# Optimization experiments

Hardware: AMD Instinct MI355X
Metric: run time of the kernel (lower is better)

The kernel has to match this reference:

```python
import jax, jax.numpy as jnp
import numpy as np

IMG = 640
C = 80
K = 10
LB, LC = 7.5, 0.5
ALPHA_COST, BETA_COST = 0.5, 6.0
GAMMA, ALPHA = 2.0, 0.25
EPS = 1e-7
PI = 3.141592653589793


def xywh_to_xyxy(b):
    cx, cy, w, h = b[..., 0], b[..., 1], b[..., 2], b[..., 3]
    return jnp.stack([cx - w * 0.5, cy - h * 0.5, cx + w * 0.5, cy + h * 0.5], axis=-1)


def bbox_iou(box1, box2):
    # box1 [M,4], box2 [N,4] xyxy -> [M,N]
    area1 = jnp.clip(box1[:, 2] - box1[:, 0], 0) * jnp.clip(box1[:, 3] - box1[:, 1], 0)
    area2 = jnp.clip(box2[:, 2] - box2[:, 0], 0) * jnp.clip(box2[:, 3] - box2[:, 1], 0)
    ix1 = jnp.maximum(box1[:, None, 0], box2[None, :, 0])
    iy1 = jnp.maximum(box1[:, None, 1], box2[None, :, 1])
    ix2 = jnp.minimum(box1[:, None, 2], box2[None, :, 2])
    iy2 = jnp.minimum(box1[:, None, 3], box2[None, :, 3])
    inter = jnp.clip(ix2 - ix1, 0) * jnp.clip(iy2 - iy1, 0)
    union = area1[:, None] + area2[None, :] - inter + EPS
    return jnp.clip(inter / union, 0.0, 1.0)


def bbox_ciou(p, t):
    # elementwise [N,4] x [N,4] xyxy -> [N]
    px1, py1, px2, py2 = p[:, 0], p[:, 1], p[:, 2], p[:, 3]
    tx1, ty1, tx2, ty2 = t[:, 0], t[:, 1], t[:, 2], t[:, 3]
    pw = jnp.clip(px2 - px1, EPS)
    ph = jnp.clip(py2 - py1, EPS)
    tw = jnp.clip(tx2 - tx1, EPS)
    th = jnp.clip(ty2 - ty1, EPS)
    inter = jnp.clip(jnp.minimum(px2, tx2) - jnp.maximum(px1, tx1), 0) * \
            jnp.clip(jnp.minimum(py2, ty2) - jnp.maximum(py1, ty1), 0)
    union = pw * ph + tw * th - inter + EPS
    iou = inter / union
    cd = ((px1 + px2) * 0.5 - (tx1 + tx2) * 0.5) ** 2 + ((py1 + py2) * 0.5 - (ty1 + ty2) * 0.5) ** 2
    cw = jnp.maximum(px2, tx2) - jnp.minimum(px1, tx1)
    ch = jnp.maximum(py2, ty2) - jnp.minimum(py1, ty1)
    c2 = cw ** 2 + ch ** 2 + EPS
    v = (4.0 / PI ** 2) * (jnp.arctan(tw / th) - jnp.arctan(pw / ph)) ** 2
    alpha = jax.lax.stop_gradient(v / (v - iou + 1.0 + EPS))
    return iou - cd / c2 - alpha * v


def _decode(p, stride):
    # p: [B, A, S, S, E] -> box [B, A*S*S, 4] (xywh px), cls [B, A*S*S, C]
    B, A, S, _, E = p.shape
    tx, ty, tw, th = p[..., 0], p[..., 1], p[..., 2], p[..., 3]
    gy, gx = jnp.meshgrid(jnp.arange(S, dtype=p.dtype), jnp.arange(S, dtype=p.dtype), indexing='ij')
    gx = gx.reshape(1, 1, S, S)
    gy = gy.reshape(1, 1, S, S)
    px = (jax.nn.sigmoid(tx) * 2.0 - 0.5 + gx) * stride  # center_mode='v8'
    py = (jax.nn.sigmoid(ty) * 2.0 - 0.5 + gy) * stride
    pw = jax.nn.softplus(tw) * stride                      # wh_mode='softplus'
    ph = jax.nn.softplus(th) * stride
    box = jnp.stack([px, py, pw, ph], axis=-1).reshape(B, -1, 4)
    cls = p[..., 4:].reshape(B, -1, C)
    return box, cls


def _per_image(p_box, p_logits, gt, labels):
    # p_box [M,4] xywh, p_logits [M,C], gt [N,4] xyxy, labels [N]
    N = gt.shape[0]
    tcx = (gt[:, 0] + gt[:, 2]) * 0.5
    tcy = (gt[:, 1] + gt[:, 3]) * 0.5
    dist = (p_box[:, 0][:, None] - tcx[None, :]) ** 2 + (p_box[:, 1][:, None] - tcy[None, :]) ** 2  # [M,N]
    _, cand = jax.lax.top_k(-dist.T, K)       # [N,K] nearest anchors per target
    cand = cand.reshape(-1)                    # [N*K] (dups don't change the min)
    cand_box = p_box[cand]
    cand_logits = p_logits[cand]
    cls_score = jax.nn.sigmoid(cand_logits)[:, labels]          # [NK,N]
    iou = bbox_iou(xywh_to_xyxy(cand_box), gt)                  # [NK,N]
    cost = ALPHA_COST * (1.0 - cls_score) + BETA_COST * (1.0 - iou)
    matched = cand[jnp.argmin(cost, axis=0)]                    # [N]
    ciou = bbox_ciou(xywh_to_xyxy(p_box[matched]), gt)
    loss_box = LB * jnp.sum(1.0 - ciou) / N
    tgt = jnp.zeros_like(p_logits).at[matched, labels].set(1.0)  # [M,C]
    x = p_logits
    ce = jnp.maximum(x, 0) - x * tgt + jnp.log1p(jnp.exp(-jnp.abs(x)))
    pr = jax.nn.sigmoid(x)
    p_t = pr * tgt + (1 - pr) * (1 - tgt)
    fl = ce * (1 - p_t) ** GAMMA
    a_t = ALPHA * tgt + (1 - ALPHA) * (1 - tgt)
    loss_cls = LC * jnp.sum(a_t * fl) / N
    return loss_box + loss_cls


def _forward(p0, p1, p2, gt_boxes, labels):
    boxes, logits = [], []
    for p in (p0, p1, p2):
        S = p.shape[2]
        pb, pl = _decode(p, float(IMG) / S)
        boxes.append(pb)
        logits.append(pl)
    flat_boxes = jnp.concatenate(boxes, axis=1)    # [B, 8400, 4]
    flat_logits = jnp.concatenate(logits, axis=1)  # [B, 8400, C]
    per_img = jax.vmap(_per_image)(flat_boxes, flat_logits, gt_boxes, labels)  # [B]
    return jnp.mean(per_img)


def setup_inputs() -> dict:
    key = jax.random.key(0)
    k0, k1, k2, kc, kw, kl = jax.random.split(key, 6)
    B, N = 16, 60
    p0 = jax.random.normal(k0, (B, 1, 80, 80, 84), dtype=jnp.float32)
    p1 = jax.random.normal(k1, (B, 1, 40, 40, 84), dtype=jnp.float32)
    p2 = jax.random.normal(k2, (B, 1, 20, 20, 84), dtype=jnp.float32)
    c = jax.random.uniform(kc, (B, N, 2), minval=64.0, maxval=576.0)
    wh = jax.random.uniform(kw, (B, N, 2), minval=8.0, maxval=128.0)
    gt_boxes = jnp.concatenate([c - wh * 0.5, c + wh * 0.5], axis=-1).astype(jnp.float32)
    labels = jax.random.randint(kl, (B, N), 0, 80, dtype=jnp.int32)
    return {"p0": p0, "p1": p1, "p2": p2, "gt_boxes": gt_boxes, "labels": labels}


def reference(p0, p1, p2, gt_boxes, labels):
    return _forward(p0, p1, p2, gt_boxes, labels)
```

## Files before the change

### kernel.cpp

```cpp
#include <hip/hip_runtime.h>
#include <cfloat>
#include <math.h>

#define NB   16
#define NGT  60
#define NA   8400
#define KNN  10
#define NCAND (NGT*KNN)
#define EPSF 1e-7f
#define PIF  3.14159265358979f

#define FOCAL_BLOCKS  2100
#define SPARSE_BLOCKS 240
#define K1_BLOCKS (FOCAL_BLOCKS + SPARSE_BLOCKS)

#define NV0   2150400u
#define NV1    537600u
#define NV2    134400u
#define FOCAL_COUNT 2688000u

#define LOG2E 1.44269504088896341f
#define LN2   0.69314718055994531f

__device__ __forceinline__ float fexp2(float x){ return __builtin_amdgcn_exp2f(x); }
__device__ __forceinline__ float flog2(float x){ return __builtin_amdgcn_logf(x); }
__device__ __forceinline__ float frcp (float x){ return __builtin_amdgcn_rcpf(x); }

__device__ __forceinline__ float fsigm(float x){
  return frcp(1.0f + fexp2(-x*LOG2E));
}
__device__ __forceinline__ float fsoftplus(float x){
  float u = fexp2(-fabsf(x)*LOG2E);
  return fmaxf(x,0.f) + LN2*flog2(1.0f + u);
}
__device__ __forceinline__ float fbg(float x){
  float u = fexp2(fminf(-x*LOG2E, 126.0f));
  float t = frcp(1.0f + u);
  return (x + LN2*flog2(1.0f + u)) * t * t;
}

__device__ __forceinline__ float focal_fbg4(const float* __restrict__ p0,
                                            const float* __restrict__ p1,
                                            const float* __restrict__ p2, unsigned u){
  unsigned g = u / 20u;
  unsigned v = 21u*g + (u - 20u*g) + 1u;
  const float* p; unsigned vloc;
  if (v < NV0)          { p=p0; vloc = v; }
  else if (v < NV0+NV1) { p=p1; vloc = v - NV0; }
  else                  { p=p2; vloc = v - (NV0+NV1); }
  float4 x4 = *(const float4*)(p + (size_t)vloc*4u);
  return fbg(x4.x) + fbg(x4.y) + fbg(x4.z) + fbg(x4.w);
}

struct ARow { const float* q; float stf; int i, j; };
__device__ __forceinline__ ARow anchor_row(const float* p0,const float* p1,const float* p2,int img,int a){
  ARow r;
  if (a < 6400){ int l=a;      r.q = p0 + (size_t)(img*6400 + l)*84; r.stf= 8.f; r.i=l/80; r.j=l-80*r.i; }
  else if (a < 8000){ int l=a-6400; r.q = p1 + (size_t)(img*1600 + l)*84; r.stf=16.f; r.i=l/40; r.j=l-40*r.i; }
  else { int l=a-8000;         r.q = p2 + (size_t)(img*400  + l)*84; r.stf=32.f; r.i=l/20; r.j=l-20*r.i; }
  return r;
}
__device__ __forceinline__ float4 decode_box_xywh(const ARow& r){
  float4 x4 = *(const float4*)r.q;
  float px = (fsigm(x4.x)*2.f - 0.5f + (float)r.j)*r.stf;
  float py = (fsigm(x4.y)*2.f - 0.5f + (float)r.i)*r.stf;
  float pw = fsoftplus(x4.z)*r.stf;
  float ph = fsoftplus(x4.w)*r.stf;
  return make_float4(px,py,pw,ph);
}

__global__ __launch_bounds__(256) void k1_kernel(const float* __restrict__ p0,
                                                 const float* __restrict__ p1,
                                                 const float* __restrict__ p2,
                                                 const float* __restrict__ gt,
                                                 const int* __restrict__ labels,
                                                 int* __restrict__ cand,
                                                 unsigned long long* __restrict__ partials,
                                                 float* __restrict__ fsum){
  if (blockIdx.x < FOCAL_BLOCKS){
    __shared__ float sbuf[4];
    const unsigned S = FOCAL_BLOCKS*256u;
    unsigned u = blockIdx.x*256u + threadIdx.x;
    float s0 = focal_fbg4(p0,p1,p2, u);
    float s1 = focal_fbg4(p0,p1,p2, u +   S);
    float s2 = focal_fbg4(p0,p1,p2, u + 2*S);
    float s3 = focal_fbg4(p0,p1,p2, u + 3*S);
    float s4 = focal_fbg4(p0,p1,p2, u + 4*S);
    float sum = (((s0 + s1) + (s2 + s3)) + s4) * 0.75f;
    #pragma unroll
    for (int off=32; off>0; off>>=1) sum += __shfl_xor(sum, off);
    int wid = threadIdx.x >> 6;
    if ((threadIdx.x & 63) == 0) sbuf[wid] = sum;
    __syncthreads();
    if (threadIdx.x == 0) fsum[blockIdx.x] = sbuf[0]+sbuf[1]+sbuf[2]+sbuf[3];
    return;
  }

  int wid  = threadIdx.x >> 6;
  int lane = threadIdx.x & 63;
  int pair = (blockIdx.x - FOCAL_BLOCKS)*4 + wid;
  int img = pair / NGT, g = pair - img*NGT;
  const float* gb = gt + (size_t)(img*NGT + g)*4;
  float tcx = (gb[0]+gb[2])*0.5f, tcy = (gb[1]+gb[3])*0.5f;

  int jx0 = (int)(tcx * 0.125f),   iy0 = (int)(tcy * 0.125f);
  int jx1 = (int)(tcx * 0.0625f),  iy1 = (int)(tcy * 0.0625f);
  int jx2 = (int)(tcx * 0.03125f), iy2 = (int)(tcy * 0.03125f);

  float d0=FLT_MAX,d1=FLT_MAX,d2=FLT_MAX,d3=FLT_MAX;
  int   a0,a1,a2,a3;
  #pragma unroll
  for (int s=0; s<4; s++){
    int c = lane + 64*s;
    float dd = FLT_MAX; int aa = 9000000 + c;
    const float* p; int i, j, S, base, rowmul, valid = 1; float stf;
    if (c < 169)      { int r=c/13,  q=c-13*r;           i=iy0-6+r; j=jx0-6+q; S=80; base=0;    p=p0; rowmul=6400; stf= 8.f; }
    else if (c < 218) { int t=c-169; int r=t/7, q=t-7*r; i=iy1-3+r; j=jx1-3+q; S=40; base=6400; p=p1; rowmul=1600; stf=16.f; }
    else if (c < 243) { int t=c-218; int r=t/5, q=t-5*r; i=iy2-2+r; j=jx2-2+q; S=20; base=8000; p=p2; rowmul=400;  stf=32.f; }
    else { valid = 0; i=j=0; S=1; base=0; p=p0; rowmul=0; stf=0.f; }
    if (valid && i>=0 && i<S && j>=0 && j<S){
      int local = i*S + j;
      const float* q4 = p + (size_t)(img*rowmul + local)*84u;
      float2 xy = *(const float2*)q4;
      float px = (fsigm(xy.x)*2.f - 0.5f + (float)j)*stf;
      float py = (fsigm(xy.y)*2.f - 0.5f + (float)i)*stf;
      float dx=px-tcx, dy=py-tcy;
      dd = dx*dx + dy*dy;
      aa = base + local;
    }
    if (s==0){ d0=dd; a0=aa; } else if (s==1){ d1=dd; a1=aa; }
    else if (s==2){ d2=dd; a2=aa; } else { d3=dd; a3=aa; }
  }

  int anc_r[KNN];
  #pragma unroll
  for (int r=0; r<KNN; r++){
    float v = d0; int anc = a0;
    if (d1 < v || (d1==v && a1<anc)){ v=d1; anc=a1; }
    if (d2 < v || (d2==v && a2<anc)){ v=d2; anc=a2; }
    if (d3 < v || (d3==v && a3<anc)){ v=d3; anc=a3; }
    #pragma unroll
    for (int off=32; off>0; off>>=1){
      float v2 = __shfl_xor(v, off);
      int  A2 = __shfl_xor(anc, off);
      if (v2 < v || (v2==v && A2<anc)){ v=v2; anc=A2; }
    }
    if (a0==anc) d0=FLT_MAX;
    if (a1==anc) d1=FLT_MAX;
    if (a2==anc) d2=FLT_MAX;
    if (a3==anc) d3=FLT_MAX;
    anc_r[r] = anc;
    if (lane == 0) cand[(size_t)pair*KNN + r] = anc;
  }

  bool jv = (lane < NGT);
  float4 gbj = make_float4(0.f,0.f,0.f,0.f);
  int labj = 0;
  if (jv){
    gbj  = *(const float4*)(gt + (size_t)(img*NGT + lane)*4);
    labj = labels[img*NGT + lane];
  }
  float a2g = fmaxf(gbj.z-gbj.x,0.f)*fmaxf(gbj.w-gbj.y,0.f);
  unsigned long long best = ~0ull;
  #pragma unroll
  for (int r=0; r<KNN; r++){
    int a = anc_r[r];
    ARow ar = anchor_row(p0,p1,p2,img,a);
    float4 b = decode_box_xywh(ar);
    float bx1=b.x-b.z*0.5f, by1=b.y-b.w*0.5f, bx2=b.x+b.z*0.5f, by2=b.y+b.w*0.5f;
    float a1 = fmaxf(bx2-bx1,0.f)*fmaxf(by2-by1,0.f);
    float ix1=fmaxf(bx1,gbj.x), iy1=fmaxf(by1,gbj.y);
    float ix2=fminf(bx2,gbj.z), iy2=fminf(by2,gbj.w);
    float inter = fmaxf(ix2-ix1,0.f)*fmaxf(iy2-iy1,0.f);
    float uni = a1 + a2g - inter + EPSF;
    float iou = fminf(fmaxf(inter/uni,0.f),1.f);
    float lg = ar.q[4+labj];
    float cost = 0.5f*(1.f - fsigm(lg)) + 6.f*(1.f - iou);
    unsigned long long pk = ((unsigned long long)__float_as_uint(cost) << 32)
                          | (unsigned)(g*KNN + r);
    if (pk < best) best = pk;
  }
  if (jv) partials[((size_t)img*NGT + g)*NGT + lane] = best;
}

__global__ __launch_bounds__(1024) void k2_kernel(const unsigned long long* __restrict__ partials,
                                                  const int* __restrict__ cand,
                                                  const float* __restrict__ gt,
                                                  const int* __restrict__ labels,
                                                  const float* __restrict__ p0,
                                                  const float* __restrict__ p1,
                                                  const float* __restrict__ p2,
                                                  const float* __restrict__ fsum,
                                                  float* __restrict__ out){
  int tid = threadIdx.x;
  int wid = tid >> 6;
  int lane = tid & 63;
  __shared__ int sm[NB][NGT];
  __shared__ int sl[NB][NGT];
  __shared__ float wb[NB], wc[NB], wf[NB];
  int img = wid;
  if (lane < NGT){
    unsigned long long best = ~0ull;
    #pragma unroll 4
    for (int g2=0; g2<NGT; g2++){
      unsigned long long v = partials[((size_t)img*NGT + g2)*NGT + lane];
      if (v < best) best = v;
    }
    int slot = (int)(best & 0xffffffffull);
    sm[img][lane] = cand[img*NCAND + slot];
    sl[img][lane] = labels[img*NGT + lane];
  }
  __syncthreads();

  float local_box = 0.f, local_corr = 0.f;
  if (lane < NGT){
    int j = lane;
    int m = sm[img][j];
    ARow ar = anchor_row(p0,p1,p2,img,m);
    float4 pb = decode_box_xywh(ar);
    float px1=pb.x-pb.z*0.5f, py1=pb.y-pb.w*0.5f, px2=pb.x+pb.z*0.5f, py2=pb.y+pb.w*0.5f;
    const float* gb = gt + (size_t)(img*NGT + j)*4;
    float gx=gb[0], gy=gb[1], gz=gb[2], gw=gb[3];
    float pw=fmaxf(px2-px1,EPSF), ph=fmaxf(py2-py1,EPSF);
    float tw=fmaxf(gz-gx,EPSF),  th=fmaxf(gw-gy,EPSF);
    float inter = fmaxf(fminf(px2,gz)-fmaxf(px1,gx),0.f)*fmaxf(fminf(py2,gw)-fmaxf(py1,gy),0.f);
    float uni = pw*ph + tw*th - inter + EPSF;
    float iou = inter/uni;
    float dcx = (px1+px2)*0.5f - (gx+gz)*0.5f;
    float dcy = (py1+py2)*0.5f - (gy+gw)*0.5f;
    float cd = dcx*dcx + dcy*dcy;
    float cw = fmaxf(px2,gz) - fminf(px1,gx);
    float ch = fmaxf(py2,gw) - fminf(py1,gy);
    float c2 = cw*cw + ch*ch + EPSF;
    float dv = atanf(tw/th) - atanf(pw/ph);
    float v  = (4.f/(PIF*PIF))*dv*dv;
    float alpha = v/(v - iou + 1.f + EPSF);
    float ciou = iou - cd/c2 - alpha*v;
    local_box = 1.f - ciou;

    int lab = sl[img][j];
    bool dup = false;
    for (int j2=0; j2<j; j2++)
      if (sm[img][j2]==m && sl[img][j2]==lab){ dup=true; break; }
    if (!dup){
      float x = ar.q[4+lab];
      float s  = fsigm(x);
      float u  = fexp2(-fabsf(x)*LOG2E);
      float lt = LN2*flog2(1.0f + u);
      float sp_pos = fmaxf(-x,0.f) + lt;
      float sp_neg = fmaxf( x,0.f) + lt;
      local_corr = 0.25f*sp_pos*(1.f-s)*(1.f-s) - 0.75f*sp_neg*s*s;
    }
  }
  float local_f = fsum[tid] + fsum[tid + 1024];
  if (tid < FOCAL_BLOCKS - 2048) local_f += fsum[tid + 2048];
  #pragma unroll
  for (int off=32; off>0; off>>=1){
    local_box  += __shfl_xor(local_box,  off);
    local_corr += __shfl_xor(local_corr, off);
    local_f    += __shfl_xor(local_f,    off);
  }
  if (lane == 0){ wb[wid]=local_box; wc[wid]=local_corr; wf[wid]=local_f; }
  __syncthreads();
  if (tid == 0){
    float sb=0.f, sc=0.f, sf=0.f;
    #pragma unroll
    for (int k=0;k<NB;k++){ sb+=wb[k]; sc+=wc[k]; sf+=wf[k]; }
    out[0] = (7.5f*sb + 0.5f*(sf + sc)) / (60.f*16.f);
  }
}

extern "C" void kernel_launch(void* const* d_in, const int* in_sizes, int n_in,
                              void* d_out, int out_size, void* d_ws, size_t ws_size,
                              hipStream_t stream){
  const float* p0 = (const float*)d_in[0];
  const float* p1 = (const float*)d_in[1];
  const float* p2 = (const float*)d_in[2];
  const float* gt = (const float*)d_in[3];
  const int* labels = (const int*)d_in[4];
  float* out = (float*)d_out;

  unsigned long long* partials = (unsigned long long*)d_ws;
  float* fsum = (float*)((char*)d_ws + (size_t)NB*NGT*NGT*8);
  int*   cand = (int*)((char*)fsum + FOCAL_BLOCKS*sizeof(float));

  k1_kernel<<<K1_BLOCKS, 256, 0, stream>>>(p0, p1, p2, gt, labels, cand, partials, fsum);
  k2_kernel<<<1, 1024, 0, stream>>>(partials, cand, gt, labels, p0, p1, p2, fsum, out);
}
```

Measured before the change: 47.54 us.

## Pack anchor index into cost key, pre-reduce per block, schedule sparse blocks first

The anchor index is encoded into the low bits of the packed cost key, so the cand buffer and its indirect lookup go away. Each sparse block reduces its four GT rows in shared memory before writing, which cuts the partials that k2 scans per image from 60 to 15. Sparse blocks are moved to the start of the grid so they are dispatched before the focal blocks and the assignment tail overlaps the streaming work. The 14-bit anchor field holds indices up to 8400, and tie-breaking stays in the same order because the slot bits sit above the anchor bits.

```diff
diff --git a/kernel.cpp b/kernel.cpp
--- a/kernel.cpp
+++ b/kernel.cpp
@@ -10,9 +10,9 @@
 #define EPSF 1e-7f
 #define PIF  3.14159265358979f
 
+#define SPARSE_BLOCKS 240
 #define FOCAL_BLOCKS  2100
-#define SPARSE_BLOCKS 240
-#define K1_BLOCKS (FOCAL_BLOCKS + SPARSE_BLOCKS)
+#define K1_BLOCKS (SPARSE_BLOCKS + FOCAL_BLOCKS)
 
 #define NV0   2150400u
 #define NV1    537600u
@@ -74,13 +74,12 @@
                                                  const float* __restrict__ p2,
                                                  const float* __restrict__ gt,
                                                  const int* __restrict__ labels,
-                                                 int* __restrict__ cand,
                                                  unsigned long long* __restrict__ partials,
                                                  float* __restrict__ fsum){
-  if (blockIdx.x < FOCAL_BLOCKS){
+  if (blockIdx.x >= SPARSE_BLOCKS){
     __shared__ float sbuf[4];
     const unsigned S = FOCAL_BLOCKS*256u;
-    unsigned u = blockIdx.x*256u + threadIdx.x;
+    unsigned u = (blockIdx.x - SPARSE_BLOCKS)*256u + threadIdx.x;
     float s0 = focal_fbg4(p0,p1,p2, u);
     float s1 = focal_fbg4(p0,p1,p2, u +   S);
     float s2 = focal_fbg4(p0,p1,p2, u + 2*S);
@@ -92,13 +91,13 @@
     int wid = threadIdx.x >> 6;
     if ((threadIdx.x & 63) == 0) sbuf[wid] = sum;
     __syncthreads();
-    if (threadIdx.x == 0) fsum[blockIdx.x] = sbuf[0]+sbuf[1]+sbuf[2]+sbuf[3];
+    if (threadIdx.x == 0) fsum[blockIdx.x - SPARSE_BLOCKS] = sbuf[0]+sbuf[1]+sbuf[2]+sbuf[3];
     return;
   }
 
   int wid  = threadIdx.x >> 6;
   int lane = threadIdx.x & 63;
-  int pair = (blockIdx.x - FOCAL_BLOCKS)*4 + wid;
+  int pair = blockIdx.x*4 + wid;
   int img = pair / NGT, g = pair - img*NGT;
   const float* gb = gt + (size_t)(img*NGT + g)*4;
   float tcx = (gb[0]+gb[2])*0.5f, tcy = (gb[1]+gb[3])*0.5f;
@@ -150,7 +149,6 @@
     if (a2==anc) d2=FLT_MAX;
     if (a3==anc) d3=FLT_MAX;
     anc_r[r] = anc;
-    if (lane == 0) cand[(size_t)pair*KNN + r] = anc;
   }
 
   bool jv = (lane < NGT);
@@ -177,14 +175,24 @@
     float lg = ar.q[4+labj];
     float cost = 0.5f*(1.f - fsigm(lg)) + 6.f*(1.f - iou);
     unsigned long long pk = ((unsigned long long)__float_as_uint(cost) << 32)
-                          | (unsigned)(g*KNN + r);
+                          | ((unsigned long long)(unsigned)(g*KNN + r) << 14)
+                          | (unsigned)a;
     if (pk < best) best = pk;
   }
-  if (jv) partials[((size_t)img*NGT + g)*NGT + lane] = best;
+
+  __shared__ unsigned long long red[4][64];
+  red[wid][lane] = best;
+  __syncthreads();
+  if (wid == 0 && jv){
+    unsigned long long b0 = red[0][lane], b1 = red[1][lane];
+    unsigned long long b2 = red[2][lane], b3 = red[3][lane];
+    unsigned long long m = b0 < b1 ? b0 : b1;
+    unsigned long long n = b2 < b3 ? b2 : b3;
+    partials[(size_t)blockIdx.x*NGT + lane] = m < n ? m : n;
+  }
 }
 
 __global__ __launch_bounds__(1024) void k2_kernel(const unsigned long long* __restrict__ partials,
-                                                  const int* __restrict__ cand,
                                                   const float* __restrict__ gt,
                                                   const int* __restrict__ labels,
                                                   const float* __restrict__ p0,
@@ -201,13 +209,12 @@
   int img = wid;
   if (lane < NGT){
     unsigned long long best = ~0ull;
-    #pragma unroll 4
-    for (int g2=0; g2<NGT; g2++){
-      unsigned long long v = partials[((size_t)img*NGT + g2)*NGT + lane];
+    #pragma unroll
+    for (int b2=0; b2<15; b2++){
+      unsigned long long v = partials[(size_t)(img*15 + b2)*NGT + lane];
       if (v < best) best = v;
     }
-    int slot = (int)(best & 0xffffffffull);
-    sm[img][lane] = cand[img*NCAND + slot];
+    sm[img][lane] = (int)(best & 0x3fffull);
     sl[img][lane] = labels[img*NGT + lane];
   }
   __syncthreads();
@@ -281,9 +288,8 @@
   float* out = (float*)d_out;
 
   unsigned long long* partials = (unsigned long long*)d_ws;
-  float* fsum = (float*)((char*)d_ws + (size_t)NB*NGT*NGT*8);
-  int*   cand = (int*)((char*)fsum + FOCAL_BLOCKS*sizeof(float));
-
-  k1_kernel<<<K1_BLOCKS, 256, 0, stream>>>(p0, p1, p2, gt, labels, cand, partials, fsum);
-  k2_kernel<<<1, 1024, 0, stream>>>(partials, cand, gt, labels, p0, p1, p2, fsum, out);
-}
+  float* fsum = (float*)((char*)d_ws + (size_t)SPARSE_BLOCKS*NGT*8);
+
+  k1_kernel<<<K1_BLOCKS, 256, 0, stream>>>(p0, p1, p2, gt, labels, partials, fsum);
+  k2_kernel<<<1, 1024, 0, stream>>>(partials, gt, labels, p0, p1, p2, fsum, out);
+}
```

After: 38.38 us, median of 2. 19.3% less time.
